# Kernel optimization log

Hardware: AMD Instinct MI355X
Metric: run time of the kernel (lower is better)

## Reference

```python
import jax, jax.numpy as jnp
import numpy as np

M, N, D = 2048, 131072, 256

def setup_inputs() -> dict:
    key = jax.random.key(0)
    kq, kv = jax.random.split(key)
    query = jax.random.normal(kq, (M, D), dtype=jnp.float32)
    vectors = jax.random.normal(kv, (N, D), dtype=jnp.float32)
    return {"query": query, "vectors": vectors}

def reference(query, vectors):
    # torch.cdist(query, vectors, p=2).argmin(dim=1)
    # Euclidean distance via ||q||^2 + ||v||^2 - 2 q.v (GEMM-based, same math)
    q_sq = jnp.sum(query * query, axis=-1, keepdims=True)        # [M,1]
    v_sq = jnp.sum(vectors * vectors, axis=-1)                    # [N]
    cross = jnp.einsum('md,nd->mn', query, vectors)               # [M,N]
    dist_sq = jnp.maximum(q_sq + v_sq[None, :] - 2.0 * cross, 0.0)
    # sqrt is monotonic so argmin(dist) == argmin(dist_sq); take sqrt for faithfulness
    dist = jnp.sqrt(dist_sq)
    return jnp.argmin(dist, axis=1)                               # [M] int
```

## Files before the change

### kernel.cpp

```cpp
#include <hip/hip_runtime.h>
#include <hip/hip_bf16.h>

#define M 2048
#define N 131072
#define D 256

#define SLICE_G 128
#define NSLICE  (N / (SLICE_G * 16))

typedef __attribute__((ext_vector_type(8))) _Float16 half8;
typedef __attribute__((ext_vector_type(8))) short short8;
typedef __attribute__((ext_vector_type(4))) float f32x4;
typedef unsigned long long ull;

__device__ __forceinline__ ull pack_key(float score, unsigned idx) {
    unsigned u = __float_as_uint(score);
    u = (u & 0x80000000u) ? ~u : (u | 0x80000000u);
    return ((ull)u << 32) | idx;
}
__device__ __forceinline__ ull shfl_xor_u64_w16(ull x, int mask) {
    unsigned lo = (unsigned)x, hi = (unsigned)(x >> 32);
    lo = (unsigned)__shfl_xor((int)lo, mask, 16);
    hi = (unsigned)__shfl_xor((int)hi, mask, 16);
    return ((ull)hi << 32) | lo;
}

__global__ __launch_bounds__(256) void convert_swz(const float* __restrict__ x,
                                                   short* __restrict__ xf,
                                                   float* __restrict__ xsq,
                                                   ull* __restrict__ keys) {
    __shared__ float part[4][16];
    const int g    = blockIdx.x;
    const int t    = threadIdx.x;
    const int w    = t >> 6;
    const int l    = t & 63;
    const int quad = (t >> 4) & 3;
    const int tx   = t & 15;

    float s = 0.f;
#pragma unroll
    for (int h = 0; h < 2; ++h) {
        const int c = w + h * 4;
        const float* src = x + (size_t)(g * 16 + tx) * D + c * 32 + quad * 8;
        float tmp[8] __attribute__((aligned(16)));
        *(float4*)&tmp[0] = *(const float4*)src;
        *(float4*)&tmp[4] = *(const float4*)(src + 4);
        half8 hh;
#pragma unroll
        for (int e = 0; e < 8; ++e) {
            hh[e] = (_Float16)tmp[e];
            s += tmp[e] * tmp[e];
        }
        *(short8*)(xf + ((size_t)g * 8 + c) * 512 + l * 8) = *(short8*)&hh;
    }
    s += __shfl_xor(s, 16, 64);
    s += __shfl_xor(s, 32, 64);
    if (l < 16) part[w][l] = s;
    __syncthreads();
    if (t < 16) xsq[g * 16 + t] = part[0][t] + part[1][t] + part[2][t] + part[3][t];
    if (keys && blockIdx.x == 0) {
        for (int i = t; i < 2 * M; i += 256) keys[i] = ~0ull;
    }
}

__global__ __launch_bounds__(256) void dist_argmin_reg(const short* __restrict__ qf,
                                                       const short* __restrict__ vf,
                                                       const float* __restrict__ vsq,
                                                       ull* __restrict__ keys1,
                                                       ull* __restrict__ keys2) {
    const int tid  = threadIdx.x;
    const int lane = tid & 63;
    const int w    = tid >> 6;
    const int tx   = lane & 15;
    const int quad = (lane >> 4) & 3;

    const int qb0 = blockIdx.x * 128 + w * 32;
    const int sg0 = blockIdx.y * SLICE_G;

    half8 aq[2][8];
#pragma unroll
    for (int mt = 0; mt < 2; ++mt)
#pragma unroll
        for (int c = 0; c < 8; ++c)
            aq[mt][c] = *(const half8*)(qf + ((size_t)((qb0 >> 4) + mt) * 8 + c) * 512 + lane * 8);

    float best_s[8];
    int   best_g[8];
#pragma unroll
    for (int i = 0; i < 8; ++i) { best_s[i] = 3.4e38f; best_g[i] = 0; }

    const short* bp = vf + ((size_t)sg0 * 8) * 512 + lane * 8;
    const float* vp = vsq + sg0 * 16 + tx;

    half8 bA[8], bB[8];
    float vA, vB;

    auto loadg = [&](half8* b, float& vs, int g) {
        const short* p = bp + (size_t)g * 4096;
#pragma unroll
        for (int c = 0; c < 8; ++c) b[c] = *(const half8*)(p + c * 512);
        vs = vp[g * 16];
    };
    auto compute = [&](const half8* b, float vsqr, int g) {
        f32x4 acc[2][2];
#pragma unroll
        for (int i = 0; i < 2; ++i) {
            acc[i][0] = (f32x4){0.f, 0.f, 0.f, 0.f};
            acc[i][1] = (f32x4){0.f, 0.f, 0.f, 0.f};
        }
#pragma unroll
        for (int c = 0; c < 8; ++c) {
            acc[0][c & 1] = __builtin_amdgcn_mfma_f32_16x16x32_f16(aq[0][c], b[c], acc[0][c & 1], 0, 0, 0);
            acc[1][c & 1] = __builtin_amdgcn_mfma_f32_16x16x32_f16(aq[1][c], b[c], acc[1][c & 1], 0, 0, 0);
        }
#pragma unroll
        for (int mt = 0; mt < 2; ++mt)
#pragma unroll
            for (int r = 0; r < 4; ++r) {
                const float sc = fmaf(-2.f, acc[mt][0][r], fmaf(-2.f, acc[mt][1][r], vsqr));
                const int s = mt * 4 + r;
                if (sc < best_s[s]) { best_s[s] = sc; best_g[s] = g; }
            }
    };

    loadg(bA, vA, 0);
    for (int g = 0; g < SLICE_G - 2; g += 2) {
        loadg(bB, vB, g + 1);
        compute(bA, vA, g);
        loadg(bA, vA, g + 2);
        compute(bB, vB, g + 1);
    }
    loadg(bB, vB, SLICE_G - 1);
    compute(bA, vA, SLICE_G - 2);
    compute(bB, vB, SLICE_G - 1);

#pragma unroll
    for (int mt = 0; mt < 2; ++mt)
#pragma unroll
        for (int r = 0; r < 4; ++r) {
            const int s = mt * 4 + r;
            const unsigned n = (unsigned)((sg0 + best_g[s]) * 16 + tx);
            ull key = pack_key(best_s[s], n);
#pragma unroll
            for (int off = 8; off; off >>= 1) {
                const ull o = shfl_xor_u64_w16(key, off);
                key = key < o ? key : o;
            }
            if (tx == 0) {
                const int row = qb0 + mt * 16 + quad * 4 + r;
                const ull old = atomicMin(&keys1[row], key);
                const ull loser = (key < old) ? old : key;
                if (loser != ~0ull) atomicMin(&keys2[row], loser);
            }
        }
}

__global__ __launch_bounds__(256) void rescore_kernel(const float* __restrict__ q,
                                                      const float* __restrict__ v,
                                                      const ull* __restrict__ keys1,
                                                      const ull* __restrict__ keys2,
                                                      int* __restrict__ out) {
    const int qi   = blockIdx.x * 4 + (threadIdx.x >> 6);
    const int lane = threadIdx.x & 63;
    const float4 qv = *(const float4*)(q + (size_t)qi * D + lane * 4);
    ull best = ~0ull;
    ull cand[2];
    cand[0] = keys1[qi];
    cand[1] = keys2[qi];
#pragma unroll
    for (int c = 0; c < 2; ++c) {
        if (cand[c] == ~0ull) continue;
        const unsigned idx = (unsigned)cand[c];
        const float4 vv = *(const float4*)(v + (size_t)idx * D + lane * 4);
        float s1 = vv.x * vv.x + vv.y * vv.y + vv.z * vv.z + vv.w * vv.w;
        float s2 = qv.x * vv.x + qv.y * vv.y + qv.z * vv.z + qv.w * vv.w;
#pragma unroll
        for (int off = 32; off; off >>= 1) {
            s1 += __shfl_xor(s1, off, 64);
            s2 += __shfl_xor(s2, off, 64);
        }
        const float dist = fmaf(-2.0f, s2, s1);
        const ull key = pack_key(dist, idx);
        best = best < key ? best : key;
    }
    if (lane == 0) out[qi] = (int)(unsigned)(best & 0xFFFFFFFFull);
}

extern "C" void kernel_launch(void* const* d_in, const int* in_sizes, int n_in,
                              void* d_out, int out_size, void* d_ws, size_t ws_size,
                              hipStream_t stream) {
    const float* q = (const float*)d_in[0];
    const float* v = (const float*)d_in[1];
    int* out = (int*)d_out;

    char* ws = (char*)d_ws;
    float* vsq = (float*)ws;                 ws += (size_t)N * sizeof(float);
    float* qsq = (float*)ws;                 ws += (size_t)M * sizeof(float);
    ull* keys1 = (ull*)ws;                   ws += (size_t)2 * M * sizeof(ull);
    ull* keys2 = keys1 + M;
    short* qf = (short*)ws;                  ws += (size_t)M * D * 2;
    short* vf = (short*)ws;

    convert_swz<<<N / 16, 256, 0, stream>>>(v, vf, vsq, nullptr);
    convert_swz<<<M / 16, 256, 0, stream>>>(q, qf, qsq, keys1);

    dim3 grid(M / 128, NSLICE);
    dist_argmin_reg<<<grid, 256, 0, stream>>>(qf, vf, vsq, keys1, keys2);

    rescore_kernel<<<M / 4, 256, 0, stream>>>(q, v, keys1, keys2, out);
}
```

Before: 366.7 us.

## Pack biased score and group index into 32-bit key, fuse conversions, remap grid per XCD

Adds a positive bias to the vector norms so every score stays positive, which lets the running argmin use one 32-bit key per slot (score with its low 6 bits replaced by the group index) instead of a float and an int. The 16-lane reduction then shuffles 32-bit values and finds the winning lane with a ballot. The two conversion launches are merged into one, and the distance grid is flattened and remapped so that contiguous vector slices land on the same XCD. SLICE_G is halved, doubling the number of slices and atomics. Truncating the score's low mantissa bits can make near-ties pick a different candidate; the top-2 rescore is meant to absorb this.

```diff
diff --git a/kernel.cpp b/kernel.cpp
--- a/kernel.cpp
+++ b/kernel.cpp
@@ -5,8 +5,9 @@
 #define N 131072
 #define D 256
 
-#define SLICE_G 128
+#define SLICE_G 64
 #define NSLICE  (N / (SLICE_G * 16))
+#define BIAS    1024.0f
 
 typedef __attribute__((ext_vector_type(8))) _Float16 half8;
 typedef __attribute__((ext_vector_type(8))) short short8;
@@ -18,19 +19,20 @@
     u = (u & 0x80000000u) ? ~u : (u | 0x80000000u);
     return ((ull)u << 32) | idx;
 }
-__device__ __forceinline__ ull shfl_xor_u64_w16(ull x, int mask) {
-    unsigned lo = (unsigned)x, hi = (unsigned)(x >> 32);
-    lo = (unsigned)__shfl_xor((int)lo, mask, 16);
-    hi = (unsigned)__shfl_xor((int)hi, mask, 16);
-    return ((ull)hi << 32) | lo;
-}
-
-__global__ __launch_bounds__(256) void convert_swz(const float* __restrict__ x,
-                                                   short* __restrict__ xf,
-                                                   float* __restrict__ xsq,
-                                                   ull* __restrict__ keys) {
+
+__global__ __launch_bounds__(256) void convert_fused(const float* __restrict__ v,
+                                                     const float* __restrict__ q,
+                                                     short* __restrict__ vf,
+                                                     short* __restrict__ qf,
+                                                     float* __restrict__ vsqb,
+                                                     ull* __restrict__ keys) {
     __shared__ float part[4][16];
-    const int g    = blockIdx.x;
+    const int b    = blockIdx.x;
+    const bool isV = (b < N / 16);
+    const int g    = isV ? b : (b - N / 16);
+    const float* x = isV ? v : q;
+    short* xf      = isV ? vf : qf;
+
     const int t    = threadIdx.x;
     const int w    = t >> 6;
     const int l    = t & 63;
@@ -53,19 +55,20 @@
         }
         *(short8*)(xf + ((size_t)g * 8 + c) * 512 + l * 8) = *(short8*)&hh;
     }
-    s += __shfl_xor(s, 16, 64);
-    s += __shfl_xor(s, 32, 64);
-    if (l < 16) part[w][l] = s;
-    __syncthreads();
-    if (t < 16) xsq[g * 16 + t] = part[0][t] + part[1][t] + part[2][t] + part[3][t];
-    if (keys && blockIdx.x == 0) {
+    if (isV) {
+        s += __shfl_xor(s, 16, 64);
+        s += __shfl_xor(s, 32, 64);
+        if (l < 16) part[w][l] = s;
+        __syncthreads();
+        if (t < 16) vsqb[g * 16 + t] = part[0][t] + part[1][t] + part[2][t] + part[3][t] + BIAS;
+    } else if (g == 0) {
         for (int i = t; i < 2 * M; i += 256) keys[i] = ~0ull;
     }
 }
 
 __global__ __launch_bounds__(256) void dist_argmin_reg(const short* __restrict__ qf,
                                                        const short* __restrict__ vf,
-                                                       const float* __restrict__ vsq,
+                                                       const float* __restrict__ vsqb,
                                                        ull* __restrict__ keys1,
                                                        ull* __restrict__ keys2) {
     const int tid  = threadIdx.x;
@@ -74,8 +77,14 @@
     const int tx   = lane & 15;
     const int quad = (lane >> 4) & 3;
 
-    const int qb0 = blockIdx.x * 128 + w * 32;
-    const int sg0 = blockIdx.y * SLICE_G;
+    const int lb    = blockIdx.x;
+    const int xcd   = lb & 7;
+    const int s_    = lb >> 3;
+    const int slice = xcd * (NSLICE / 8) + (s_ >> 4);
+    const int qblk  = s_ & 15;
+
+    const int qb0 = qblk * 128 + w * 32;
+    const int sg0 = slice * SLICE_G;
 
     half8 aq[2][8];
 #pragma unroll
@@ -84,13 +93,12 @@
         for (int c = 0; c < 8; ++c)
             aq[mt][c] = *(const half8*)(qf + ((size_t)((qb0 >> 4) + mt) * 8 + c) * 512 + lane * 8);
 
-    float best_s[8];
-    int   best_g[8];
-#pragma unroll
-    for (int i = 0; i < 8; ++i) { best_s[i] = 3.4e38f; best_g[i] = 0; }
+    unsigned best[8];
+#pragma unroll
+    for (int i = 0; i < 8; ++i) best[i] = 0xFFFFFFFFu;
 
     const short* bp = vf + ((size_t)sg0 * 8) * 512 + lane * 8;
-    const float* vp = vsq + sg0 * 16 + tx;
+    const float* vp = vsqb + sg0 * 16 + tx;
 
     half8 bA[8], bB[8];
     float vA, vB;
@@ -118,8 +126,9 @@
 #pragma unroll
             for (int r = 0; r < 4; ++r) {
                 const float sc = fmaf(-2.f, acc[mt][0][r], fmaf(-2.f, acc[mt][1][r], vsqr));
-                const int s = mt * 4 + r;
-                if (sc < best_s[s]) { best_s[s] = sc; best_g[s] = g; }
+                const unsigned key = (__float_as_uint(sc) & 0xFFFFFFC0u) | (unsigned)g;
+                const int sl = mt * 4 + r;
+                best[sl] = key < best[sl] ? key : best[sl];
             }
     };
 
@@ -138,18 +147,22 @@
     for (int mt = 0; mt < 2; ++mt)
 #pragma unroll
         for (int r = 0; r < 4; ++r) {
-            const int s = mt * 4 + r;
-            const unsigned n = (unsigned)((sg0 + best_g[s]) * 16 + tx);
-            ull key = pack_key(best_s[s], n);
+            const int sl = mt * 4 + r;
+            unsigned k = best[sl];
 #pragma unroll
             for (int off = 8; off; off >>= 1) {
-                const ull o = shfl_xor_u64_w16(key, off);
-                key = key < o ? key : o;
+                const unsigned o = (unsigned)__shfl_xor((int)k, off, 16);
+                k = o < k ? o : k;
             }
+            const ull bal = __ballot(best[sl] == k);
+            const unsigned grp = (unsigned)((bal >> (quad * 16)) & 0xFFFFull);
+            const int wtx = __ffs((int)grp) - 1;
+            const unsigned n = (unsigned)((sg0 + (int)(k & 63u)) * 16 + wtx);
             if (tx == 0) {
                 const int row = qb0 + mt * 16 + quad * 4 + r;
-                const ull old = atomicMin(&keys1[row], key);
-                const ull loser = (key < old) ? old : key;
+                const ull key64 = ((ull)k << 32) | n;
+                const ull old = atomicMin(&keys1[row], key64);
+                const ull loser = (key64 < old) ? old : key64;
                 if (loser != ~0ull) atomicMin(&keys2[row], loser);
             }
         }
@@ -194,18 +207,15 @@
     int* out = (int*)d_out;
 
     char* ws = (char*)d_ws;
-    float* vsq = (float*)ws;                 ws += (size_t)N * sizeof(float);
-    float* qsq = (float*)ws;                 ws += (size_t)M * sizeof(float);
+    float* vsqb = (float*)ws;                ws += (size_t)N * sizeof(float);
     ull* keys1 = (ull*)ws;                   ws += (size_t)2 * M * sizeof(ull);
     ull* keys2 = keys1 + M;
     short* qf = (short*)ws;                  ws += (size_t)M * D * 2;
     short* vf = (short*)ws;
 
-    convert_swz<<<N / 16, 256, 0, stream>>>(v, vf, vsq, nullptr);
-    convert_swz<<<M / 16, 256, 0, stream>>>(q, qf, qsq, keys1);
-
-    dim3 grid(M / 128, NSLICE);
-    dist_argmin_reg<<<grid, 256, 0, stream>>>(qf, vf, vsq, keys1, keys2);
+    convert_fused<<<N / 16 + M / 16, 256, 0, stream>>>(v, q, vf, qf, vsqb, keys1);
+
+    dist_argmin_reg<<<16 * NSLICE, 256, 0, stream>>>(qf, vf, vsqb, keys1, keys2);
 
     rescore_kernel<<<M / 4, 256, 0, stream>>>(q, v, keys1, keys2, out);
 }
```

After: 355.1 us. 3.2% less time.
